# Kernel tuning notes

Hardware: AMD Instinct MI355X
Metric: run time of the kernel (lower is better)

## Reference

```python
import jax, jax.numpy as jnp
import numpy as np

N_NODES = 50000
N_EDGES = 800000
D = 64
N_LAYERS = 3  # layer_dims = [64, 64, 64, 64]


def setup_inputs() -> dict:
    key = jax.random.key(0)
    ks = jax.random.split(key, 5)
    x = jax.random.normal(ks[0], (N_NODES, D), dtype=jnp.float32)
    edge_index = jax.random.randint(ks[1], (2, N_EDGES), 0, N_NODES, dtype=jnp.int64)
    scale = 1.0 / np.sqrt(D)
    # Per-layer restriction (message) maps, self-loop maps, and biases.
    W_msg = jax.random.normal(ks[2], (N_LAYERS, D, D), dtype=jnp.float32) * scale
    W_self = jax.random.normal(ks[3], (N_LAYERS, D, D), dtype=jnp.float32) * scale
    b = jax.random.normal(ks[4], (N_LAYERS, D), dtype=jnp.float32) * 0.01
    return {"x": x, "edge_index": edge_index, "W_msg": W_msg, "W_self": W_self, "b": b}


def reference(x, edge_index, W_msg, W_self, b):
    """Stacked sheaf conv layers: per-edge gather -> linear restriction ->
    scatter-sum aggregation to destination nodes + self-loop linear + bias,
    with ReLU between layers (none after the final layer)."""
    n = x.shape[0]
    src, dst = edge_index[0], edge_index[1]
    n_layers = W_msg.shape[0]
    for i in range(n_layers):
        msg = x[src] @ W_msg[i]                                   # [E, d] gather + restriction
        agg = jax.ops.segment_sum(msg, dst, num_segments=n)       # [N, d] scatter-add
        x = x @ W_self[i] + agg + b[i]                            # self-loop + aggregate + bias
        if i < n_layers - 1:
            x = jax.nn.relu(x)
    return x
```

## Files before the change

kernel.cpp:

```cpp
#include <hip/hip_runtime.h>

#define D 64

__device__ __forceinline__ unsigned short f2bf(float f) {
    unsigned u = __float_as_uint(f);
    unsigned r = (u + 0x7FFFu + ((u >> 16) & 1u)) >> 16;
    return (unsigned short)r;
}
__device__ __forceinline__ float bf2f(unsigned short h) {
    return __uint_as_float((unsigned)h << 16);
}

typedef __attribute__((ext_vector_type(8))) short bf16x8;
typedef __attribute__((ext_vector_type(4))) float f32x4;

__global__ void prep_kernel(const float* __restrict__ x, unsigned short* __restrict__ xb,
                            int total, int* __restrict__ deg, int N,
                            const float* __restrict__ Wself,
                            const float* __restrict__ Wmsg,
                            unsigned short* __restrict__ Bt, int n_layers,
                            int* __restrict__ dhist) {
    int i = blockIdx.x * blockDim.x + threadIdx.x;
    if (i < N) deg[i] = 0;
    if (i < 1024) dhist[i] = 0;
    int wtotal = n_layers * D * 2 * D;
    if (i < wtotal) {
        int k = i & 127;
        int n = (i >> 7) & 63;
        int l = i >> 13;
        float w = (k < D) ? Wself[(size_t)l * D * D + k * D + n]
                          : Wmsg [(size_t)l * D * D + (k - D) * D + n];
        unsigned short hi = f2bf(w);
        unsigned short lo = f2bf(w - bf2f(hi));
        size_t base = (size_t)l * 2 * D * 2 * D;
        Bt[base + (size_t)n * 128 + k] = hi;
        Bt[base + 8192 + (size_t)n * 128 + k] = lo;
    }
    int base = i * 4;
    if (base + 4 <= total) {
        float4 v = *reinterpret_cast<const float4*>(x + base);
        ushort4 o;
        o.x = f2bf(v.x); o.y = f2bf(v.y); o.z = f2bf(v.z); o.w = f2bf(v.w);
        *reinterpret_cast<ushort4*>(xb + base) = o;
    } else if (base < total) {
        for (int k = base; k < total; ++k) xb[k] = f2bf(x[k]);
    }
}

__global__ void hist_rank_kernel(const int* __restrict__ dst, int* __restrict__ deg,
                                 int* __restrict__ rank, int E) {
    int i = blockIdx.x * blockDim.x + threadIdx.x;
    int base = i * 8;
    if (base + 8 <= E) {
        int4 d0 = *reinterpret_cast<const int4*>(dst + base);
        int4 d1 = *reinterpret_cast<const int4*>(dst + base + 4);
        int4 r0, r1;
        r0.x = atomicAdd(&deg[d0.x], 1);
        r0.y = atomicAdd(&deg[d0.y], 1);
        r0.z = atomicAdd(&deg[d0.z], 1);
        r0.w = atomicAdd(&deg[d0.w], 1);
        r1.x = atomicAdd(&deg[d1.x], 1);
        r1.y = atomicAdd(&deg[d1.y], 1);
        r1.z = atomicAdd(&deg[d1.z], 1);
        r1.w = atomicAdd(&deg[d1.w], 1);
        *reinterpret_cast<int4*>(rank + base) = r0;
        *reinterpret_cast<int4*>(rank + base + 4) = r1;
    } else {
        for (int e = base; e < E; ++e) rank[e] = atomicAdd(&deg[dst[e]], 1);
    }
}

__global__ void scan_k1(const int* __restrict__ deg, int* __restrict__ bsum, int n,
                        int* __restrict__ dhist) {
    __shared__ int sh[256];
    __shared__ int lh[1024];
    int t = threadIdx.x;
    for (int i = t; i < 1024; i += 256) lh[i] = 0;
    __syncthreads();
    int g = blockIdx.x * 256 + t;
    int v = (g < n) ? deg[g] : 0;
    if (g < n) atomicAdd(&lh[min(v, 1023)], 1);
    sh[t] = v;
    __syncthreads();
    for (int off = 1; off < 256; off <<= 1) {
        int u = (t >= off) ? sh[t - off] : 0;
        __syncthreads();
        sh[t] += u;
        __syncthreads();
    }
    if (t == 255) bsum[blockIdx.x] = sh[255];
    __syncthreads();
    for (int i = t; i < 1024; i += 256) {
        int c = lh[i];
        if (c) atomicAdd(&dhist[i], c);
    }
}

__global__ void scan_k2(const int* __restrict__ bsum, int* __restrict__ boff, int nb,
                        const int* __restrict__ dhist, int* __restrict__ dbase) {
    __shared__ int sh[1024];
    int t = threadIdx.x;
    int v = (t < nb) ? bsum[t] : 0;
    sh[t] = v;
    __syncthreads();
    for (int off = 1; off < 1024; off <<= 1) {
        int u = (t >= off) ? sh[t - off] : 0;
        __syncthreads();
        sh[t] += u;
        __syncthreads();
    }
    if (t < nb) boff[t] = sh[t] - v;
    __syncthreads();
    int rb = 1023 - t;
    int dv = dhist[rb];
    sh[t] = dv;
    __syncthreads();
    for (int off = 1; off < 1024; off <<= 1) {
        int u = (t >= off) ? sh[t - off] : 0;
        __syncthreads();
        sh[t] += u;
        __syncthreads();
    }
    dbase[rb] = sh[t] - dv;
}

__global__ void scan_k3(const int* __restrict__ deg, const int* __restrict__ boff,
                        int* __restrict__ row_ptr, int n) {
    __shared__ int sh[256];
    int t = threadIdx.x;
    int g = blockIdx.x * 256 + t;
    int v = (g < n) ? deg[g] : 0;
    sh[t] = v;
    __syncthreads();
    for (int off = 1; off < 256; off <<= 1) {
        int u = (t >= off) ? sh[t - off] : 0;
        __syncthreads();
        sh[t] += u;
        __syncthreads();
    }
    if (g < n) {
        int excl = sh[t] - v + boff[blockIdx.x];
        row_ptr[g] = excl;
        if (g == n - 1) row_ptr[n] = excl + v;
    }
}

__global__ void perm_nodes_kernel(const int* __restrict__ deg, int* __restrict__ dbase,
                                  int* __restrict__ nperm, int N) {
    __shared__ int lh[1024];
    __shared__ int lbase[1024];
    int t = threadIdx.x;
    for (int i = t; i < 1024; i += 256) lh[i] = 0;
    __syncthreads();
    int n = blockIdx.x * 256 + t;
    int b = 0, lrank = 0;
    if (n < N) {
        b = min(deg[n], 1023);
        lrank = atomicAdd(&lh[b], 1);
    }
    __syncthreads();
    for (int i = t; i < 1024; i += 256) {
        int c = lh[i];
        lbase[i] = c ? atomicAdd(&dbase[i], c) : 0;
    }
    __syncthreads();
    if (n < N) nperm[lbase[b] + lrank] = n;
}

__global__ void perm_rank_kernel(const int* __restrict__ src, const int* __restrict__ dst,
                                 const int* __restrict__ rank, const int* __restrict__ row_ptr,
                                 int* __restrict__ sorted_src, int E) {
    int i = blockIdx.x * blockDim.x + threadIdx.x;
    int base = i * 8;
    if (base + 8 <= E) {
        int4 d0 = *reinterpret_cast<const int4*>(dst + base);
        int4 d1 = *reinterpret_cast<const int4*>(dst + base + 4);
        int4 s0 = *reinterpret_cast<const int4*>(src + base);
        int4 s1 = *reinterpret_cast<const int4*>(src + base + 4);
        int4 r0 = *reinterpret_cast<const int4*>(rank + base);
        int4 r1 = *reinterpret_cast<const int4*>(rank + base + 4);
        int p0 = row_ptr[d0.x] + r0.x;
        int p1 = row_ptr[d0.y] + r0.y;
        int p2 = row_ptr[d0.z] + r0.z;
        int p3 = row_ptr[d0.w] + r0.w;
        int p4 = row_ptr[d1.x] + r1.x;
        int p5 = row_ptr[d1.y] + r1.y;
        int p6 = row_ptr[d1.z] + r1.z;
        int p7 = row_ptr[d1.w] + r1.w;
        __builtin_nontemporal_store(s0.x, &sorted_src[p0]);
        __builtin_nontemporal_store(s0.y, &sorted_src[p1]);
        __builtin_nontemporal_store(s0.z, &sorted_src[p2]);
        __builtin_nontemporal_store(s0.w, &sorted_src[p3]);
        __builtin_nontemporal_store(s1.x, &sorted_src[p4]);
        __builtin_nontemporal_store(s1.y, &sorted_src[p5]);
        __builtin_nontemporal_store(s1.z, &sorted_src[p6]);
        __builtin_nontemporal_store(s1.w, &sorted_src[p7]);
    } else {
        for (int e = base; e < E; ++e)
            sorted_src[row_ptr[dst[e]] + rank[e]] = src[e];
    }
}

__device__ __forceinline__ void acc16(float* ac, uint4 u0, uint4 u1) {
    ac[0]  += __uint_as_float(u0.x << 16);
    ac[1]  += __uint_as_float(u0.x & 0xFFFF0000u);
    ac[2]  += __uint_as_float(u0.y << 16);
    ac[3]  += __uint_as_float(u0.y & 0xFFFF0000u);
    ac[4]  += __uint_as_float(u0.z << 16);
    ac[5]  += __uint_as_float(u0.z & 0xFFFF0000u);
    ac[6]  += __uint_as_float(u0.w << 16);
    ac[7]  += __uint_as_float(u0.w & 0xFFFF0000u);
    ac[8]  += __uint_as_float(u1.x << 16);
    ac[9]  += __uint_as_float(u1.x & 0xFFFF0000u);
    ac[10] += __uint_as_float(u1.y << 16);
    ac[11] += __uint_as_float(u1.y & 0xFFFF0000u);
    ac[12] += __uint_as_float(u1.z << 16);
    ac[13] += __uint_as_float(u1.z & 0xFFFF0000u);
    ac[14] += __uint_as_float(u1.w << 16);
    ac[15] += __uint_as_float(u1.w & 0xFFFF0000u);
}

__global__ void __launch_bounds__(256)
fused_layer(const unsigned short* __restrict__ xb,
            const int* __restrict__ row_ptr,
            const int* __restrict__ sorted_src,
            const int* __restrict__ nperm,
            const unsigned short* __restrict__ Bt,
            const float* __restrict__ bias,
            float* __restrict__ out_f32,
            unsigned short* __restrict__ out_bf16,
            int n_nodes, int E, int last) {
    __shared__ float red[4][16][68];
    __shared__ int snode[16];

    int lane = threadIdx.x & 63;
    int w    = threadIdx.x >> 6;
    int ln15 = lane & 15;
    int lhi  = lane >> 4;

    int node0 = blockIdx.x << 4;
    int slot  = node0 + ln15;
    int scl   = min(slot, n_nodes - 1);
    int node  = nperm[scl];
    if (lane < 16) snode[lane] = node;

    int beg = row_ptr[node];
    int end = row_ptr[node + 1];
    if (slot >= n_nodes) end = beg;
    int deg = end - beg;

    int md = deg;
    md = max(md, __shfl_xor(md, 1));
    md = max(md, __shfl_xor(md, 2));
    md = max(md, __shfl_xor(md, 4));
    md = max(md, __shfl_xor(md, 8));

    float ac[16];
#pragma unroll
    for (int t = 0; t < 16; ++t) ac[t] = 0.f;

    const int Em1 = E - 1;
    int p = w;
    for (; p + 4 < md; p += 8) {
        int cA = min(beg + p,     Em1);
        int cB = min(beg + p + 4, Em1);
        int sA = sorted_src[cA];
        int sB = sorted_src[cB];
        const unsigned short* rA = xb + (((size_t)(unsigned)sA) << 6) + (lhi << 3);
        const unsigned short* rB = xb + (((size_t)(unsigned)sB) << 6) + (lhi << 3);
        uint4 a0 = *reinterpret_cast<const uint4*>(rA);
        uint4 a1 = *reinterpret_cast<const uint4*>(rA + 32);
        uint4 b0 = *reinterpret_cast<const uint4*>(rB);
        uint4 b1 = *reinterpret_cast<const uint4*>(rB + 32);
        if (p < deg)     acc16(ac, a0, a1);
        if (p + 4 < deg) acc16(ac, b0, b1);
    }
    for (; p < md; p += 4) {
        int cA = min(beg + p, Em1);
        int sA = sorted_src[cA];
        const unsigned short* rA = xb + (((size_t)(unsigned)sA) << 6) + (lhi << 3);
        uint4 a0 = *reinterpret_cast<const uint4*>(rA);
        uint4 a1 = *reinterpret_cast<const uint4*>(rA + 32);
        if (p < deg) acc16(ac, a0, a1);
    }

    int f0 = lhi << 3;
    *reinterpret_cast<float4*>(&red[w][ln15][f0])      = make_float4(ac[0], ac[1], ac[2], ac[3]);
    *reinterpret_cast<float4*>(&red[w][ln15][f0 + 4])  = make_float4(ac[4], ac[5], ac[6], ac[7]);
    *reinterpret_cast<float4*>(&red[w][ln15][32 + f0]) = make_float4(ac[8], ac[9], ac[10], ac[11]);
    *reinterpret_cast<float4*>(&red[w][ln15][36 + f0]) = make_float4(ac[12], ac[13], ac[14], ac[15]);

    bf16x8 Bf[2][4];
    {
        const unsigned short* bp = Bt + ((size_t)(w * 16 + ln15)) * 128 + (lhi << 3);
#pragma unroll
        for (int pp = 0; pp < 2; ++pp)
#pragma unroll
            for (int kc = 0; kc < 4; ++kc)
                Bf[pp][kc] = *reinterpret_cast<const bf16x8*>(bp + pp * 8192 + kc * 32);
    }
    const unsigned short* xr = xb + (((size_t)(unsigned)node) << 6) + (lhi << 3);
    bf16x8 A0 = *reinterpret_cast<const bf16x8*>(xr);
    bf16x8 A1 = *reinterpret_cast<const bf16x8*>(xr + 32);
    float bb = bias[w * 16 + ln15];

    __syncthreads();

    float s[16];
#pragma unroll
    for (int t = 0; t < 16; ++t) s[t] = 0.f;
#pragma unroll
    for (int ww = 0; ww < 4; ++ww) {
        float4 r0 = *reinterpret_cast<const float4*>(&red[ww][ln15][f0]);
        float4 r1 = *reinterpret_cast<const float4*>(&red[ww][ln15][f0 + 4]);
        float4 r2 = *reinterpret_cast<const float4*>(&red[ww][ln15][32 + f0]);
        float4 r3 = *reinterpret_cast<const float4*>(&red[ww][ln15][36 + f0]);
        s[0]  += r0.x; s[1]  += r0.y; s[2]  += r0.z; s[3]  += r0.w;
        s[4]  += r1.x; s[5]  += r1.y; s[6]  += r1.z; s[7]  += r1.w;
        s[8]  += r2.x; s[9]  += r2.y; s[10] += r2.z; s[11] += r2.w;
        s[12] += r3.x; s[13] += r3.y; s[14] += r3.z; s[15] += r3.w;
    }
    bf16x8 A2, A3;
#pragma unroll
    for (int t = 0; t < 8; ++t) A2[t] = (short)f2bf(s[t]);
#pragma unroll
    for (int t = 0; t < 8; ++t) A3[t] = (short)f2bf(s[8 + t]);

    f32x4 c = {0.f, 0.f, 0.f, 0.f};
    c = __builtin_amdgcn_mfma_f32_16x16x32_bf16(A0, Bf[0][0], c, 0, 0, 0);
    c = __builtin_amdgcn_mfma_f32_16x16x32_bf16(A0, Bf[1][0], c, 0, 0, 0);
    c = __builtin_amdgcn_mfma_f32_16x16x32_bf16(A1, Bf[0][1], c, 0, 0, 0);
    c = __builtin_amdgcn_mfma_f32_16x16x32_bf16(A1, Bf[1][1], c, 0, 0, 0);
    c = __builtin_amdgcn_mfma_f32_16x16x32_bf16(A2, Bf[0][2], c, 0, 0, 0);
    c = __builtin_amdgcn_mfma_f32_16x16x32_bf16(A2, Bf[1][2], c, 0, 0, 0);
    c = __builtin_amdgcn_mfma_f32_16x16x32_bf16(A3, Bf[0][3], c, 0, 0, 0);
    c = __builtin_amdgcn_mfma_f32_16x16x32_bf16(A3, Bf[1][3], c, 0, 0, 0);

    int colo = w * 16 + ln15;
    if (last) {
#pragma unroll
        for (int r = 0; r < 4; ++r) {
            int sl = lhi * 4 + r;
            if (node0 + sl < n_nodes) {
                int nr = snode[sl];
                out_f32[((size_t)(unsigned)nr << 6) + colo] = c[r] + bb;
            }
        }
    } else {
#pragma unroll
        for (int r = 0; r < 4; ++r) {
            int sl = lhi * 4 + r;
            if (node0 + sl < n_nodes) {
                int nr = snode[sl];
                out_bf16[((size_t)(unsigned)nr << 6) + colo] = f2bf(fmaxf(c[r] + bb, 0.f));
            }
        }
    }
}

__global__ void scatter_kernel(const float* __restrict__ x,
                               const int* __restrict__ src,
                               const int* __restrict__ dst,
                               float* __restrict__ agg, int n_edges) {
    int e = blockIdx.x * (blockDim.x >> 6) + (threadIdx.x >> 6);
    int lane = threadIdx.x & 63;
    if (e >= n_edges) return;
    float v = x[(size_t)src[e] * D + lane];
    unsafeAtomicAdd(&agg[(size_t)dst[e] * D + lane], v);
}

__global__ void dense_kernel(const float* __restrict__ xin,
                             const float* __restrict__ agg,
                             const float* __restrict__ Wself,
                             const float* __restrict__ Wmsg,
                             const float* __restrict__ bias,
                             float* __restrict__ xout,
                             int n_nodes, int do_relu) {
    __shared__ float Ws[D * D];
    __shared__ float Wm[D * D];
    for (int i = threadIdx.x; i < D * D; i += blockDim.x) {
        Ws[i] = Wself[i];
        Wm[i] = Wmsg[i];
    }
    __syncthreads();
    int lane = threadIdx.x & 63;
    int wave = threadIdx.x >> 6;
    int wpb = blockDim.x >> 6;
    float bj = bias[lane];
    for (int n = blockIdx.x * wpb + wave; n < n_nodes; n += gridDim.x * wpb) {
        float xv = xin[(size_t)n * D + lane];
        float av = agg[(size_t)n * D + lane];
        float acc = bj;
#pragma unroll
        for (int k = 0; k < D; ++k) {
            acc += __shfl(xv, k, 64) * Ws[k * D + lane]
                 + __shfl(av, k, 64) * Wm[k * D + lane];
        }
        if (do_relu) acc = fmaxf(acc, 0.f);
        xout[(size_t)n * D + lane] = acc;
    }
}

extern "C" void kernel_launch(void* const* d_in, const int* in_sizes, int n_in,
                              void* d_out, int out_size, void* d_ws, size_t ws_size,
                              hipStream_t stream) {
    const float* x0    = (const float*)d_in[0];
    const int*   ei    = (const int*)d_in[1];
    const float* Wmsg  = (const float*)d_in[2];
    const float* Wself = (const float*)d_in[3];
    const float* bias  = (const float*)d_in[4];
    float* out = (float*)d_out;

    const int N = in_sizes[0] / D;
    const int E = in_sizes[1] / 2;
    const int n_layers = in_sizes[4] / D;

    const int* src = ei;
    const int* dst = ei + E;
    const size_t NB = (size_t)N * D * sizeof(float);

    const int NBB = (N + 255) / 256;
    const size_t BtB = (size_t)n_layers * 2 * D * 2 * D * 2;
    const size_t need = (size_t)N * D * 2
                      + (size_t)N * D * 2
                      + BtB
                      + (size_t)E * 4
                      + (size_t)E * 4
                      + (size_t)(N + 1) * 4
                      + (size_t)N * 4
                      + (size_t)N * 4
                      + 1024 * 4 * 2
                      + (size_t)NBB * 4 * 2 + 256;

    if (ws_size >= need && NBB <= 1024) {
        char* p = (char*)d_ws;
        unsigned short* Xb   = (unsigned short*)p;  p += (size_t)N * D * 2;
        unsigned short* Xb2  = (unsigned short*)p;  p += (size_t)N * D * 2;
        unsigned short* Bt   = (unsigned short*)p;  p += BtB;
        int* sorted_src      = (int*)p;             p += (size_t)E * 4;
        int* rank            = (int*)p;             p += (size_t)E * 4;
        int* row_ptr         = (int*)p;             p += (size_t)(N + 1) * 4;
        int* deg             = (int*)p;             p += (size_t)N * 4;
        int* nperm           = (int*)p;             p += (size_t)N * 4;
        int* dhist           = (int*)p;             p += 1024 * 4;
        int* dbase           = (int*)p;             p += 1024 * 4;
        int* bsum            = (int*)p;             p += (size_t)NBB * 4;
        int* boff            = (int*)p;

        {
            int total = N * D;
            int nthr = (total + 3) / 4;
            prep_kernel<<<(nthr + 255) / 256, 256, 0, stream>>>(
                x0, Xb, total, deg, N, Wself, Wmsg, Bt, n_layers, dhist);

            int threads = 256;
            int nthr8 = (E + 7) / 8;
            int blocks = (nthr8 + threads - 1) / threads;
            hist_rank_kernel<<<blocks, threads, 0, stream>>>(dst, deg, rank, E);
            scan_k1<<<NBB, 256, 0, stream>>>(deg, bsum, N, dhist);
            scan_k2<<<1, 1024, 0, stream>>>(bsum, boff, NBB, dhist, dbase);
            scan_k3<<<NBB, 256, 0, stream>>>(deg, boff, row_ptr, N);
            perm_nodes_kernel<<<NBB, 256, 0, stream>>>(deg, dbase, nperm, N);
            perm_rank_kernel<<<blocks, threads, 0, stream>>>(src, dst, rank, row_ptr,
                                                             sorted_src, E);
        }

        const int dtiles = (N + 15) >> 4;
        const unsigned short* in_b = Xb;
        unsigned short* out_b = Xb2;

        for (int layer = 0; layer < n_layers; ++layer) {
            fused_layer<<<dtiles, 256, 0, stream>>>(
                in_b, row_ptr, sorted_src, nperm,
                Bt + (size_t)layer * 2 * D * 2 * D,
                bias + (size_t)layer * D,
                out, out_b, N, E, (layer == n_layers - 1) ? 1 : 0);
            const unsigned short* t = in_b;
            in_b = out_b;
            out_b = (unsigned short*)t;
        }
    } else {
        float* agg = (float*)d_ws;
        const int EPB = 256 / 64;
        const int scatter_blocks = (E + EPB - 1) / EPB;
        for (int layer = 0; layer < n_layers; ++layer) {
            hipMemsetAsync(agg, 0, NB, stream);
            const float* xin = (layer == 0) ? x0 : out;
            scatter_kernel<<<scatter_blocks, 256, 0, stream>>>(xin, src, dst, agg, E);
            dense_kernel<<<1024, 256, 0, stream>>>(
                xin, agg,
                Wself + (size_t)layer * D * D,
                Wmsg  + (size_t)layer * D * D,
                bias  + (size_t)layer * D,
                out, N, (layer < n_layers - 1) ? 1 : 0);
        }
    }
}
```

Before: 248.6 us.

## Stage neighbor indices in LDS and gather four neighbors per iteration

Before gathering, the block now cooperatively loads up to 64 source indices per node into shared memory with coalesced reads, so the gather loop reads indices from LDS instead of issuing a dependent global index load ahead of each row fetch. The gather loop is also widened to issue four neighbor row loads per iteration, raising memory-level parallelism. The cost is an extra staging phase with two added barriers, more LDS use that may lower occupancy, and a slow global fallback path for nodes with degree above the cap.

```diff
diff --git a/kernel.cpp b/kernel.cpp
--- a/kernel.cpp
+++ b/kernel.cpp
@@ -1,6 +1,7 @@
 #include <hip/hip_runtime.h>
 
 #define D 64
+#define IDXCAP 64
 
 __device__ __forceinline__ unsigned short f2bf(float f) {
     unsigned u = __float_as_uint(f);
@@ -231,57 +232,90 @@
             unsigned short* __restrict__ out_bf16,
             int n_nodes, int E, int last) {
     __shared__ float red[4][16][68];
+    __shared__ int idx[IDXCAP][17];
     __shared__ int snode[16];
-
-    int lane = threadIdx.x & 63;
-    int w    = threadIdx.x >> 6;
+    __shared__ int sbeg[16];
+    __shared__ int sdeg[16];
+
+    int t    = threadIdx.x;
+    int lane = t & 63;
+    int w    = t >> 6;
     int ln15 = lane & 15;
     int lhi  = lane >> 4;
 
     int node0 = blockIdx.x << 4;
-    int slot  = node0 + ln15;
-    int scl   = min(slot, n_nodes - 1);
-    int node  = nperm[scl];
-    if (lane < 16) snode[lane] = node;
-
-    int beg = row_ptr[node];
-    int end = row_ptr[node + 1];
-    if (slot >= n_nodes) end = beg;
-    int deg = end - beg;
-
-    int md = deg;
-    md = max(md, __shfl_xor(md, 1));
-    md = max(md, __shfl_xor(md, 2));
-    md = max(md, __shfl_xor(md, 4));
-    md = max(md, __shfl_xor(md, 8));
+    if (t < 16) {
+        int slot = node0 + t;
+        int scl  = min(slot, n_nodes - 1);
+        int nd   = nperm[scl];
+        snode[t] = nd;
+        int b  = row_ptr[nd];
+        int e2 = row_ptr[nd + 1];
+        if (slot >= n_nodes) e2 = b;
+        sbeg[t] = b;
+        sdeg[t] = e2 - b;
+    }
+    __syncthreads();
+
+    int md = 0;
+#pragma unroll
+    for (int i = 0; i < 16; ++i) md = max(md, sdeg[i]);
+    int mdc = min(md, IDXCAP);
+
+    {
+        int sn = t >> 4;
+        int sj = t & 15;
+        int sb = sbeg[sn];
+        int sd = sdeg[sn];
+        for (int jj = sj; jj < mdc; jj += 16)
+            idx[jj][sn] = (jj < sd) ? sorted_src[sb + jj] : 0;
+    }
+    __syncthreads();
+
+    int beg = sbeg[ln15];
+    int deg = sdeg[ln15];
+    int node = snode[ln15];
 
     float ac[16];
 #pragma unroll
-    for (int t = 0; t < 16; ++t) ac[t] = 0.f;
+    for (int q = 0; q < 16; ++q) ac[q] = 0.f;
 
     const int Em1 = E - 1;
-    int p = w;
-    for (; p + 4 < md; p += 8) {
-        int cA = min(beg + p,     Em1);
-        int cB = min(beg + p + 4, Em1);
-        int sA = sorted_src[cA];
-        int sB = sorted_src[cB];
-        const unsigned short* rA = xb + (((size_t)(unsigned)sA) << 6) + (lhi << 3);
-        const unsigned short* rB = xb + (((size_t)(unsigned)sB) << 6) + (lhi << 3);
-        uint4 a0 = *reinterpret_cast<const uint4*>(rA);
-        uint4 a1 = *reinterpret_cast<const uint4*>(rA + 32);
-        uint4 b0 = *reinterpret_cast<const uint4*>(rB);
-        uint4 b1 = *reinterpret_cast<const uint4*>(rB + 32);
-        if (p < deg)     acc16(ac, a0, a1);
-        if (p + 4 < deg) acc16(ac, b0, b1);
-    }
-    for (; p < md; p += 4) {
-        int cA = min(beg + p, Em1);
-        int sA = sorted_src[cA];
-        const unsigned short* rA = xb + (((size_t)(unsigned)sA) << 6) + (lhi << 3);
-        uint4 a0 = *reinterpret_cast<const uint4*>(rA);
-        uint4 a1 = *reinterpret_cast<const uint4*>(rA + 32);
-        if (p < deg) acc16(ac, a0, a1);
+    int mdcm1 = (mdc > 0) ? mdc - 1 : 0;
+    for (int pos = w; pos < md; pos += 16) {
+        int p0 = pos, p1 = pos + 4, p2 = pos + 8, p3 = pos + 12;
+        int s0, s1, s2, s3;
+        if (p3 < mdc) {
+            s0 = idx[p0][ln15];
+            s1 = idx[p1][ln15];
+            s2 = idx[p2][ln15];
+            s3 = idx[p3][ln15];
+        } else {
+            s0 = (p0 < mdc) ? idx[min(p0, mdcm1)][ln15]
+                            : ((p0 < md) ? sorted_src[min(beg + p0, Em1)] : 0);
+            s1 = (p1 < mdc) ? idx[min(p1, mdcm1)][ln15]
+                            : ((p1 < md) ? sorted_src[min(beg + p1, Em1)] : 0);
+            s2 = (p2 < mdc) ? idx[min(p2, mdcm1)][ln15]
+                            : ((p2 < md) ? sorted_src[min(beg + p2, Em1)] : 0);
+            s3 = (p3 < mdc) ? idx[min(p3, mdcm1)][ln15]
+                            : ((p3 < md) ? sorted_src[min(beg + p3, Em1)] : 0);
+        }
+        const unsigned short* r0 = xb + (((size_t)(unsigned)s0) << 6) + (lhi << 3);
+        const unsigned short* r1 = xb + (((size_t)(unsigned)s1) << 6) + (lhi << 3);
+        const unsigned short* r2 = xb + (((size_t)(unsigned)s2) << 6) + (lhi << 3);
+        const unsigned short* r3 = xb + (((size_t)(unsigned)s3) << 6) + (lhi << 3);
+        uint4 a0 = *reinterpret_cast<const uint4*>(r0);
+        uint4 a1 = *reinterpret_cast<const uint4*>(r0 + 32);
+        uint4 b0 = *reinterpret_cast<const uint4*>(r1);
+        uint4 b1 = *reinterpret_cast<const uint4*>(r1 + 32);
+        uint4 c0 = *reinterpret_cast<const uint4*>(r2);
+        uint4 c1 = *reinterpret_cast<const uint4*>(r2 + 32);
+        uint4 d0 = *reinterpret_cast<const uint4*>(r3);
+        uint4 d1 = *reinterpret_cast<const uint4*>(r3 + 32);
+        if (p0 < deg) acc16(ac, a0, a1);
+        if (p1 < deg) acc16(ac, b0, b1);
+        if (p2 < deg) acc16(ac, c0, c1);
+        if (p3 < deg) acc16(ac, d0, d1);
     }
 
     int f0 = lhi << 3;
@@ -308,7 +342,7 @@
 
     float s[16];
 #pragma unroll
-    for (int t = 0; t < 16; ++t) s[t] = 0.f;
+    for (int q = 0; q < 16; ++q) s[q] = 0.f;
 #pragma unroll
     for (int ww = 0; ww < 4; ++ww) {
         float4 r0 = *reinterpret_cast<const float4*>(&red[ww][ln15][f0]);
@@ -322,9 +356,9 @@
     }
     bf16x8 A2, A3;
 #pragma unroll
-    for (int t = 0; t < 8; ++t) A2[t] = (short)f2bf(s[t]);
-#pragma unroll
-    for (int t = 0; t < 8; ++t) A3[t] = (short)f2bf(s[8 + t]);
+    for (int q = 0; q < 8; ++q) A2[q] = (short)f2bf(s[q]);
+#pragma unroll
+    for (int q = 0; q < 8; ++q) A3[q] = (short)f2bf(s[8 + q]);
 
     f32x4 c = {0.f, 0.f, 0.f, 0.f};
     c = __builtin_amdgcn_mfma_f32_16x16x32_bf16(A0, Bf[0][0], c, 0, 0, 0);
```

After: 256.0 us. 3.0% more time.
